# Performance work log

Hardware: AMD Instinct MI355X
Metric: run time of the kernel (lower is better)

Reference implementation:

```python
import jax, jax.numpy as jnp
import numpy as np


def _quat_to_rot(q):
    # q: [B,4] (w,x,y,z); normalize as the torch code does when norm != 1
    q = q / jnp.linalg.norm(q, axis=-1, keepdims=True)
    w, x, y, z = q[:, 0], q[:, 1], q[:, 2], q[:, 3]
    r00 = 1 - 2 * y**2 - 2 * z**2
    r01 = 2 * x * y - 2 * z * w
    r02 = 2 * x * z + 2 * y * w
    r10 = 2 * x * y + 2 * z * w
    r11 = 1 - 2 * x**2 - 2 * z**2
    r12 = 2 * y * z - 2 * x * w
    r20 = 2 * x * z - 2 * y * w
    r21 = 2 * y * z + 2 * x * w
    r22 = 1 - 2 * x**2 - 2 * y**2
    R = jnp.stack([
        jnp.stack([r00, r01, r02], axis=-1),
        jnp.stack([r10, r11, r12], axis=-1),
        jnp.stack([r20, r21, r22], axis=-1),
    ], axis=-2)  # [B,3,3]
    return R


def setup_inputs() -> dict:
    key = jax.random.key(0)
    k1, k2, k3, k4 = jax.random.split(key, 4)
    B, N = 32, 262144
    return {
        "pcd_mis": jax.random.normal(k1, (B, N, 3), dtype=jnp.float32),
        "T_mis": jax.random.normal(k2, (B, 4, 4), dtype=jnp.float32),
        "delta_q_pred": jax.random.normal(k3, (B, 4), dtype=jnp.float32),
        "delta_t_pred": jax.random.normal(k4, (B, 3), dtype=jnp.float32),
    }


def reference(pcd_mis, T_mis, delta_q_pred, delta_t_pred):
    B = delta_q_pred.shape[0]
    R = _quat_to_rot(delta_q_pred)                      # [B,3,3]
    t = delta_t_pred[:, :, None]                        # [B,3,1]
    top = jnp.concatenate([R, t], axis=-1)              # [B,3,4]
    bottom = jnp.broadcast_to(
        jnp.array([0.0, 0.0, 0.0, 1.0], dtype=pcd_mis.dtype), (B, 1, 4))
    delta_T = jnp.concatenate([top, bottom], axis=-2)   # [B,4,4]
    inv_T = jnp.linalg.inv(delta_T)                     # [B,4,4]
    batch_T_pred = jnp.einsum('bij,bjk->bik', inv_T, T_mis)  # [B,4,4]
    # homogeneous point transform: only first 3 output rows are kept
    # new = (inv_T @ [p;1])[:3] = p @ Rinv^T + tinv
    pcd_new = jnp.einsum('bij,bnj->bni', inv_T[:, :3, :3], pcd_mis) \
        + inv_T[:, None, :3, 3]                          # [B,N,3]
    return (batch_T_pred, pcd_new)
```

## Files before the change

kernel.cpp:

```cpp
#include <hip/hip_runtime.h>
#include <math.h>

struct Inv {
    float i00, i01, i02, it0;
    float i10, i11, i12, it1;
    float i20, i21, i22, it2;
};

__device__ __forceinline__ Inv make_inv(const float* __restrict__ q,
                                        const float* __restrict__ t, int b) {
    float w = q[b * 4 + 0], x = q[b * 4 + 1], y = q[b * 4 + 2], z = q[b * 4 + 3];
    float inv_n = 1.0f / sqrtf(w * w + x * x + y * y + z * z);
    w *= inv_n; x *= inv_n; y *= inv_n; z *= inv_n;
    float R00 = 1.f - 2.f * y * y - 2.f * z * z;
    float R01 = 2.f * x * y - 2.f * z * w;
    float R02 = 2.f * x * z + 2.f * y * w;
    float R10 = 2.f * x * y + 2.f * z * w;
    float R11 = 1.f - 2.f * x * x - 2.f * z * z;
    float R12 = 2.f * y * z - 2.f * x * w;
    float R20 = 2.f * x * z - 2.f * y * w;
    float R21 = 2.f * y * z + 2.f * x * w;
    float R22 = 1.f - 2.f * x * x - 2.f * y * y;
    float t0 = t[b * 3 + 0], t1 = t[b * 3 + 1], t2 = t[b * 3 + 2];
    Inv v;
    v.i00 = R00; v.i01 = R10; v.i02 = R20; v.it0 = -(R00 * t0 + R10 * t1 + R20 * t2);
    v.i10 = R01; v.i11 = R11; v.i12 = R21; v.it1 = -(R01 * t0 + R11 * t1 + R21 * t2);
    v.i20 = R02; v.i21 = R12; v.i22 = R22; v.it2 = -(R02 * t0 + R12 * t1 + R22 * t2);
    return v;
}

__device__ __forceinline__ void xf(const Inv& M, float px, float py, float pz,
                                   float& ox, float& oy, float& oz) {
    ox = fmaf(M.i00, px, fmaf(M.i01, py, fmaf(M.i02, pz, M.it0)));
    oy = fmaf(M.i10, px, fmaf(M.i11, py, fmaf(M.i12, pz, M.it1)));
    oz = fmaf(M.i20, px, fmaf(M.i21, py, fmaf(M.i22, pz, M.it2)));
}

__global__ void tmat_kernel(const float* __restrict__ T_mis,
                            const float* __restrict__ q,
                            const float* __restrict__ t,
                            float* __restrict__ out, int total) {
    int tid = blockIdx.x * blockDim.x + threadIdx.x;
    if (tid >= total) return;
    int b = tid >> 4;
    int i = (tid >> 2) & 3;
    int j = tid & 3;
    const float* Tb = T_mis + b * 16;
    float val;
    if (i < 3) {
        Inv M = make_inv(q, t, b);
        float a0, a1, a2, it;
        if (i == 0)      { a0 = M.i00; a1 = M.i01; a2 = M.i02; it = M.it0; }
        else if (i == 1) { a0 = M.i10; a1 = M.i11; a2 = M.i12; it = M.it1; }
        else             { a0 = M.i20; a1 = M.i21; a2 = M.i22; it = M.it2; }
        val = fmaf(a0, Tb[0 * 4 + j],
              fmaf(a1, Tb[1 * 4 + j],
              fmaf(a2, Tb[2 * 4 + j],
                   it * Tb[3 * 4 + j])));
    } else {
        val = Tb[3 * 4 + j];
    }
    out[tid] = val;
}

__global__ __launch_bounds__(256) void pcd_kernel(const float4* __restrict__ pcd,
                                                  const float* __restrict__ q,
                                                  const float* __restrict__ t,
                                                  float4* __restrict__ out,
                                                  int f4_per_batch) {
    const int b = blockIdx.y;
    Inv M = make_inv(q, t, b);
    const size_t g = (size_t)blockIdx.x * blockDim.x + threadIdx.x;
    const size_t base = (size_t)b * (size_t)f4_per_batch + g * 3u;
    float4 v0 = pcd[base + 0];
    float4 v1 = pcd[base + 1];
    float4 v2 = pcd[base + 2];
    float4 o0, o1, o2;
    xf(M, v0.x, v0.y, v0.z, o0.x, o0.y, o0.z);
    xf(M, v0.w, v1.x, v1.y, o0.w, o1.x, o1.y);
    xf(M, v1.z, v1.w, v2.x, o1.z, o1.w, o2.x);
    xf(M, v2.y, v2.z, v2.w, o2.y, o2.z, o2.w);
    out[base + 0] = o0;
    out[base + 1] = o1;
    out[base + 2] = o2;
}

extern "C" void kernel_launch(void* const* d_in, const int* in_sizes, int n_in,
                              void* d_out, int out_size, void* d_ws, size_t ws_size,
                              hipStream_t stream) {
    const float* pcd   = (const float*)d_in[0];
    const float* T_mis = (const float*)d_in[1];
    const float* q     = (const float*)d_in[2];
    const float* t     = (const float*)d_in[3];
    float* out = (float*)d_out;

    const int B = in_sizes[2] / 4;
    const long long N = (long long)in_sizes[0] / (3LL * B);

    {
        int total = B * 16;
        int threads = 256;
        int blocks = (total + threads - 1) / threads;
        tmat_kernel<<<blocks, threads, 0, stream>>>(T_mis, q, t, out, total);
    }

    {
        const int f4_per_batch = (int)(3 * N / 4);
        const int groups_per_batch = (int)(N / 4);
        const int threads = 256;
        dim3 grid(groups_per_batch / threads, B);
        pcd_kernel<<<grid, threads, 0, stream>>>((const float4*)pcd, q, t,
                                                 (float4*)(out + B * 16), f4_per_batch);
    }
}
```

Measured before the change: 189.3 us.

## Fuse matrix kernel into point kernel and stage points through LDS for coalescing

Merges the small 4x4 matrix kernel into the point-transform kernel, so block 0 of each batch also writes the batch transform and one launch is removed. Point loads and stores now go through shared memory: each thread reads and writes contiguous float4s across the block, and the 3-float4 per-thread regrouping happens in LDS. This aims to make global accesses fully coalesced instead of stride-3 float4 per lane. The cost is two barriers and LDS traffic, with stride-3 float4 LDS accesses that may cause bank conflicts.

```diff
diff --git a/kernel.cpp b/kernel.cpp
--- a/kernel.cpp
+++ b/kernel.cpp
@@ -36,53 +36,68 @@
     oz = fmaf(M.i20, px, fmaf(M.i21, py, fmaf(M.i22, pz, M.it2)));
 }
 
-__global__ void tmat_kernel(const float* __restrict__ T_mis,
-                            const float* __restrict__ q,
-                            const float* __restrict__ t,
-                            float* __restrict__ out, int total) {
-    int tid = blockIdx.x * blockDim.x + threadIdx.x;
-    if (tid >= total) return;
-    int b = tid >> 4;
-    int i = (tid >> 2) & 3;
-    int j = tid & 3;
-    const float* Tb = T_mis + b * 16;
-    float val;
-    if (i < 3) {
-        Inv M = make_inv(q, t, b);
-        float a0, a1, a2, it;
-        if (i == 0)      { a0 = M.i00; a1 = M.i01; a2 = M.i02; it = M.it0; }
-        else if (i == 1) { a0 = M.i10; a1 = M.i11; a2 = M.i12; it = M.it1; }
-        else             { a0 = M.i20; a1 = M.i21; a2 = M.i22; it = M.it2; }
-        val = fmaf(a0, Tb[0 * 4 + j],
-              fmaf(a1, Tb[1 * 4 + j],
-              fmaf(a2, Tb[2 * 4 + j],
-                   it * Tb[3 * 4 + j])));
-    } else {
-        val = Tb[3 * 4 + j];
+__global__ __launch_bounds__(256) void realign_fused_kernel(
+        const float4* __restrict__ pcd,
+        const float* __restrict__ T_mis,
+        const float* __restrict__ q,
+        const float* __restrict__ t,
+        float* __restrict__ out_mat,
+        float4* __restrict__ out_pcd,
+        int f4_per_batch) {
+    __shared__ float4 smem[768];
+    const int b = blockIdx.y;
+    const int tid = threadIdx.x;
+    const size_t chunk = (size_t)b * (size_t)f4_per_batch + (size_t)blockIdx.x * 768u;
+
+    float4 r0 = pcd[chunk + tid];
+    float4 r1 = pcd[chunk + 256 + tid];
+    float4 r2 = pcd[chunk + 512 + tid];
+
+    const Inv M = make_inv(q, t, b);
+
+    smem[tid]       = r0;
+    smem[256 + tid] = r1;
+    smem[512 + tid] = r2;
+
+    if (blockIdx.x == 0 && tid < 16) {
+        const int i = tid >> 2;
+        const int j = tid & 3;
+        const float* Tb = T_mis + b * 16;
+        float val;
+        if (i < 3) {
+            float a0, a1, a2, it;
+            if (i == 0)      { a0 = M.i00; a1 = M.i01; a2 = M.i02; it = M.it0; }
+            else if (i == 1) { a0 = M.i10; a1 = M.i11; a2 = M.i12; it = M.it1; }
+            else             { a0 = M.i20; a1 = M.i21; a2 = M.i22; it = M.it2; }
+            val = fmaf(a0, Tb[0 * 4 + j],
+                  fmaf(a1, Tb[1 * 4 + j],
+                  fmaf(a2, Tb[2 * 4 + j],
+                       it * Tb[3 * 4 + j])));
+        } else {
+            val = Tb[3 * 4 + j];
+        }
+        out_mat[b * 16 + tid] = val;
     }
-    out[tid] = val;
-}
 
-__global__ __launch_bounds__(256) void pcd_kernel(const float4* __restrict__ pcd,
-                                                  const float* __restrict__ q,
-                                                  const float* __restrict__ t,
-                                                  float4* __restrict__ out,
-                                                  int f4_per_batch) {
-    const int b = blockIdx.y;
-    Inv M = make_inv(q, t, b);
-    const size_t g = (size_t)blockIdx.x * blockDim.x + threadIdx.x;
-    const size_t base = (size_t)b * (size_t)f4_per_batch + g * 3u;
-    float4 v0 = pcd[base + 0];
-    float4 v1 = pcd[base + 1];
-    float4 v2 = pcd[base + 2];
+    __syncthreads();
+
+    float4 v0 = smem[3 * tid + 0];
+    float4 v1 = smem[3 * tid + 1];
+    float4 v2 = smem[3 * tid + 2];
     float4 o0, o1, o2;
     xf(M, v0.x, v0.y, v0.z, o0.x, o0.y, o0.z);
     xf(M, v0.w, v1.x, v1.y, o0.w, o1.x, o1.y);
     xf(M, v1.z, v1.w, v2.x, o1.z, o1.w, o2.x);
     xf(M, v2.y, v2.z, v2.w, o2.y, o2.z, o2.w);
-    out[base + 0] = o0;
-    out[base + 1] = o1;
-    out[base + 2] = o2;
+    smem[3 * tid + 0] = o0;
+    smem[3 * tid + 1] = o1;
+    smem[3 * tid + 2] = o2;
+
+    __syncthreads();
+
+    out_pcd[chunk + tid]       = smem[tid];
+    out_pcd[chunk + 256 + tid] = smem[256 + tid];
+    out_pcd[chunk + 512 + tid] = smem[512 + tid];
 }
 
 extern "C" void kernel_launch(void* const* d_in, const int* in_sizes, int n_in,
@@ -96,20 +111,11 @@
 
     const int B = in_sizes[2] / 4;
     const long long N = (long long)in_sizes[0] / (3LL * B);
+    const int f4_per_batch = (int)(3 * N / 4);
+    const int blocks_x = f4_per_batch / 768;
 
-    {
-        int total = B * 16;
-        int threads = 256;
-        int blocks = (total + threads - 1) / threads;
-        tmat_kernel<<<blocks, threads, 0, stream>>>(T_mis, q, t, out, total);
-    }
-
-    {
-        const int f4_per_batch = (int)(3 * N / 4);
-        const int groups_per_batch = (int)(N / 4);
-        const int threads = 256;
-        dim3 grid(groups_per_batch / threads, B);
-        pcd_kernel<<<grid, threads, 0, stream>>>((const float4*)pcd, q, t,
-                                                 (float4*)(out + B * 16), f4_per_batch);
-    }
+    dim3 grid(blocks_x, B);
+    realign_fused_kernel<<<grid, 256, 0, stream>>>(
+        (const float4*)pcd, T_mis, q, t,
+        out, (float4*)(out + B * 16), f4_per_batch);
 }
```

Result: faster. 180.2 us (-4.8%).
